# Kernel tuning notes

Measured on AMD Instinct MI355X. Metric: run time of the kernel, lower is better.

The kernel has to match this reference:

```python
import jax, jax.numpy as jnp
import numpy as np

B, T, C, E = 16, 392, 512, 512
E8 = E // 8          # dim_project output
K = T // 2           # top_k / number of sampled positions
RECEPTIVE_FIELD = 2.0


def setup_inputs() -> dict:
    key = jax.random.key(0)
    ks = jax.random.split(key, 6)
    s = 0.03  # trunc_normal std used by the module init
    return {
        "x_in": jax.random.normal(ks[0], (B, T, C), jnp.float32),
        "W_dim": jax.random.normal(ks[1], (E8, E), jnp.float32) * s,
        "b_dim": jnp.zeros((E8,), jnp.float32),
        "W_time": jax.random.normal(ks[2], (T, T * T), jnp.float32) * s,
        "b_time": jnp.zeros((T,), jnp.float32),
        "W_offa": jax.random.normal(ks[3], (K, T), jnp.float32) * s,
        "W_offd": jax.random.normal(ks[4], (K, T), jnp.float32) * s,
    }


def _grid_sample_1d(x, idx_norm):
    """Bilinear 1D sample along last axis of x (b,T,c) at normalized coords
    idx_norm (b,K); padding_mode='border', align_corners=False.
    Equivalent to the module's F.grid_sample on (b,T,c,1) with grid (0, g)."""
    c = x.shape[-1]
    ix = ((idx_norm + 1.0) * c - 1.0) * 0.5          # unnormalize (align_corners=False)
    x0 = jnp.floor(ix)
    w1 = ix - x0                                     # fractional weight
    x0i = jnp.clip(x0.astype(jnp.int32), 0, c - 1)   # border clamp
    x1i = jnp.clip(x0.astype(jnp.int32) + 1, 0, c - 1)
    v0 = jnp.take_along_axis(x, x0i[:, None, :], axis=2)  # (b,T,K)
    v1 = jnp.take_along_axis(x, x1i[:, None, :], axis=2)
    return v0 * (1.0 - w1)[:, None, :] + v1 * w1[:, None, :]


def reference(x_in, W_dim, b_dim, W_time, b_time, W_offa, W_offd):
    b, t, c = x_in.shape
    scaler = 1.0 / E
    # dot-similarity attention map
    xi = jnp.einsum('btc,ec->bte', x_in, W_dim) + b_dim          # (b,t,E8)
    att = jax.nn.softmax(scaler * jnp.einsum('bie,bje->bij', xi, xi), axis=-1)
    # giant time projection: (b, t*t) @ (t*t, t)
    xt = att.reshape(b, t * t) @ W_time.T + b_time               # (b,t)
    off_a = jnp.tanh(xt @ W_offa.T) * RECEPTIVE_FIELD            # (b,K)
    off_d = jnp.tanh(xt @ W_offd.T) * RECEPTIVE_FIELD
    idx_a = jnp.arange(0, t, 2, dtype=jnp.float32)[None, :] + off_a
    idx_d = jnp.arange(1, t + 1, 2, dtype=jnp.float32)[None, :] + off_d
    # normalize_grid: n = K*2 = t
    denom = float(max(t - 1, 1))
    g_a = 2.0 * idx_a / denom - 1.0
    g_d = 2.0 * idx_d / denom - 1.0
    x_a = _grid_sample_1d(x_in, g_a)                             # (b,t,K)
    x_d = _grid_sample_1d(x_in, g_d)
    return (x_a, x_d)
```

## Files before the change

kernel.cpp:

```cpp
#include <hip/hip_runtime.h>
#include <hip/hip_bf16.h>

constexpr int BB   = 16;
constexpr int TT_  = 392;
constexpr int CC   = 512;
constexpr int E8_  = 64;
constexpr int KK   = 196;
constexpr long TT2 = 153664;
constexpr long OUT_HALF = 1229312;

constexpr int NC2 = 98;
constexpr int CH2 = 1568;
constexpr int NJT16 = 25;

constexpr int LDA = 68;

typedef __bf16 bf16_t;
typedef bf16_t bf16x8 __attribute__((ext_vector_type(8)));
typedef float  f32x4  __attribute__((ext_vector_type(4)));

static __device__ __forceinline__ unsigned int pk2(float a, float b) {
    unsigned short lo = __builtin_bit_cast(unsigned short, (bf16_t)a);
    unsigned short hi = __builtin_bit_cast(unsigned short, (bf16_t)b);
    return ((unsigned int)hi << 16) | (unsigned int)lo;
}
static __device__ __forceinline__ bf16x8 cvt8(f32x4 a, f32x4 b) {
    uint4 u = make_uint4(pk2(a.x, a.y), pk2(a.z, a.w), pk2(b.x, b.y), pk2(b.z, b.w));
    return __builtin_bit_cast(bf16x8, u);
}
static __device__ __forceinline__ bf16x8 ld_frag(const bf16_t* p) {
    uint2 lo = *(const uint2*)p;
    uint2 hi = *(const uint2*)(p + 4);
    uint4 u = make_uint4(lo.x, lo.y, hi.x, hi.y);
    return __builtin_bit_cast(bf16x8, u);
}

__global__ __launch_bounds__(256) void k_xi(const float* __restrict__ x,
                                            const float* __restrict__ Wd,
                                            const float* __restrict__ bd,
                                            unsigned short* __restrict__ xi_b,
                                            float* __restrict__ xt) {
    int tid = threadIdx.x;
    if (blockIdx.x < 25) {
        int o = blockIdx.x * 256 + tid;
        if (o < BB * TT_) xt[o] = 0.f;
    }
    int wv = tid >> 6, lane = tid & 63;
    int n = lane & 15, quad = lane >> 4;
    int m = blockIdx.x * 64 + wv * 16 + n;
    const float* xp = x  + (size_t)m * CC + quad * 8;
    const float* wp = Wd + (size_t)n * CC + quad * 8;

    f32x4 acc[4] = {};
    f32x4 a0c, a1c, b0c[4], b1c[4];
    a0c = *(const f32x4*)xp;
    a1c = *(const f32x4*)(xp + 4);
    #pragma unroll
    for (int nt = 0; nt < 4; ++nt) {
        b0c[nt] = *(const f32x4*)(wp + (size_t)nt * 16 * CC);
        b1c[nt] = *(const f32x4*)(wp + (size_t)nt * 16 * CC + 4);
    }
    for (int kt = 0; kt < 16; ++kt) {
        f32x4 a0n, a1n, b0n[4], b1n[4];
        if (kt < 15) {
            a0n = *(const f32x4*)(xp + (kt + 1) * 32);
            a1n = *(const f32x4*)(xp + (kt + 1) * 32 + 4);
            #pragma unroll
            for (int nt = 0; nt < 4; ++nt) {
                b0n[nt] = *(const f32x4*)(wp + (size_t)nt * 16 * CC + (kt + 1) * 32);
                b1n[nt] = *(const f32x4*)(wp + (size_t)nt * 16 * CC + (kt + 1) * 32 + 4);
            }
        }
        bf16x8 a = cvt8(a0c, a1c);
        #pragma unroll
        for (int nt = 0; nt < 4; ++nt) {
            bf16x8 b = cvt8(b0c[nt], b1c[nt]);
            acc[nt] = __builtin_amdgcn_mfma_f32_16x16x32_bf16(a, b, acc[nt], 0, 0, 0);
        }
        if (kt < 15) {
            a0c = a0n; a1c = a1n;
            #pragma unroll
            for (int nt = 0; nt < 4; ++nt) { b0c[nt] = b0n[nt]; b1c[nt] = b1n[nt]; }
        }
    }
    #pragma unroll
    for (int nt = 0; nt < 4; ++nt)
        #pragma unroll
        for (int r = 0; r < 4; ++r) {
            int mm = blockIdx.x * 64 + wv * 16 + quad * 4 + r;
            int e = nt * 16 + n;
            xi_b[(size_t)mm * E8_ + e] =
                __builtin_bit_cast(unsigned short, (bf16_t)(acc[nt][r] + bd[e]));
        }
}

__global__ __launch_bounds__(256) void k_att(const unsigned short* __restrict__ xi_b,
                                             unsigned short* __restrict__ att_b) {
    __shared__ bf16_t Xb[400 * LDA];
    int b = blockIdx.x, tb = blockIdx.y;
    int tid = threadIdx.x;
    int wv = tid >> 6, lane = tid & 63;
    int n = lane & 15, quad = lane >> 4;
    #pragma unroll
    for (int t = 0; t < 13; ++t) {
        int s = t * 256 + tid;
        if (s < 3200) {
            int r = s >> 3, c8 = s & 7;
            uint2 lo = make_uint2(0u, 0u), hi = make_uint2(0u, 0u);
            if (r < TT_) {
                uint4 v = *(const uint4*)(xi_b + ((size_t)(b * TT_ + r)) * E8_ + c8 * 8);
                lo = make_uint2(v.x, v.y);
                hi = make_uint2(v.z, v.w);
            }
            *(uint2*)(&Xb[r * LDA + c8 * 8])     = lo;
            *(uint2*)(&Xb[r * LDA + c8 * 8 + 4]) = hi;
        }
    }
    __syncthreads();
    int arow = tb * 64 + wv * 16 + n;
    if (arow > 399) arow = 399;
    bf16x8 a0 = ld_frag(&Xb[arow * LDA + quad * 8]);
    bf16x8 a1 = ld_frag(&Xb[arow * LDA + 32 + quad * 8]);
    f32x4 acc[25];
    #pragma unroll
    for (int nt = 0; nt < 25; ++nt) acc[nt] = (f32x4){0.f, 0.f, 0.f, 0.f};
    #pragma unroll
    for (int nt = 0; nt < 25; ++nt) {
        bf16x8 b0 = ld_frag(&Xb[(nt * 16 + n) * LDA + quad * 8]);
        bf16x8 b1 = ld_frag(&Xb[(nt * 16 + n) * LDA + 32 + quad * 8]);
        acc[nt] = __builtin_amdgcn_mfma_f32_16x16x32_bf16(a0, b0, acc[nt], 0, 0, 0);
        acc[nt] = __builtin_amdgcn_mfma_f32_16x16x32_bf16(a1, b1, acc[nt], 0, 0, 0);
    }
    const float scaler = 1.0f / 512.0f;
    float mx[4] = {-1e30f, -1e30f, -1e30f, -1e30f};
    #pragma unroll
    for (int nt = 0; nt < 25; ++nt) {
        bool valid = (nt * 16 + n) < TT_;
        #pragma unroll
        for (int r = 0; r < 4; ++r) {
            float v = valid ? acc[nt][r] * scaler : -1e30f;
            acc[nt][r] = v;
            mx[r] = fmaxf(mx[r], v);
        }
    }
    #pragma unroll
    for (int r = 0; r < 4; ++r) {
        #pragma unroll
        for (int o = 1; o < 16; o <<= 1) mx[r] = fmaxf(mx[r], __shfl_xor(mx[r], o, 64));
    }
    float sm[4] = {0.f, 0.f, 0.f, 0.f};
    #pragma unroll
    for (int nt = 0; nt < 25; ++nt)
        #pragma unroll
        for (int r = 0; r < 4; ++r) {
            float e = __expf(acc[nt][r] - mx[r]);
            acc[nt][r] = e;
            sm[r] += e;
        }
    #pragma unroll
    for (int r = 0; r < 4; ++r) {
        #pragma unroll
        for (int o = 1; o < 16; o <<= 1) sm[r] += __shfl_xor(sm[r], o, 64);
        sm[r] = 1.0f / sm[r];
    }
    unsigned short* dst = att_b + (size_t)b * TT2;
    #pragma unroll
    for (int r = 0; r < 4; ++r) {
        int ti = tb * 64 + wv * 16 + quad * 4 + r;
        if (ti < TT_) {
            #pragma unroll
            for (int nt = 0; nt < 25; ++nt) {
                int tj = nt * 16 + n;
                if (tj < TT_)
                    dst[(size_t)ti * TT_ + tj] =
                        __builtin_bit_cast(unsigned short, (bf16_t)(acc[nt][r] * sm[r]));
            }
        }
    }
}

__global__ __launch_bounds__(256) void k_xt(const float* __restrict__ Wt,
                                            const unsigned short* __restrict__ att_b,
                                            float* __restrict__ xt) {
    int wg = blockIdx.x;
    int xcd = wg & 7, s = wg >> 3;
    int cidx = s / 7, jt4 = s - cidx * 7;
    int c = cidx * 8 + xcd;
    if (c >= NC2) return;
    int tid = threadIdx.x;
    int wv = tid >> 6, lane = tid & 63;
    int n = lane & 15, quad = lane >> 4;
    int jt = jt4 * 4 + wv;
    if (jt >= NJT16) return;
    int j = jt * 16 + n;
    int jl = j < TT_ ? j : TT_ - 1;
    long kbase = (long)c * CH2;
    const unsigned short* ap = att_b + (size_t)n * TT2 + kbase + quad * 8;
    const float*          wp = Wt + (size_t)jl * TT2 + kbase + quad * 8;

    f32x4 acc = {0.f, 0.f, 0.f, 0.f};
    uint4 ac; f32x4 w0c, w1c;
    ac  = *(const uint4*)ap;
    w0c = *(const f32x4*)wp;
    w1c = *(const f32x4*)(wp + 4);
    for (int m = 0; m < 49; ++m) {
        uint4 an; f32x4 w0n, w1n;
        if (m < 48) {
            ac.w = ac.w;
            an  = *(const uint4*)(ap + (m + 1) * 32);
            w0n = *(const f32x4*)(wp + (m + 1) * 32);
            w1n = *(const f32x4*)(wp + (m + 1) * 32 + 4);
        }
        bf16x8 a = __builtin_bit_cast(bf16x8, ac);
        bf16x8 b = cvt8(w0c, w1c);
        acc = __builtin_amdgcn_mfma_f32_16x16x32_bf16(a, b, acc, 0, 0, 0);
        if (m < 48) { ac = an; w0c = w0n; w1c = w1n; }
    }
    if (j < TT_) {
        #pragma unroll
        for (int r = 0; r < 4; ++r)
            unsafeAtomicAdd(&xt[(size_t)(quad * 4 + r) * TT_ + j], acc[r]);
    }
}

__global__ __launch_bounds__(256) void k_off(const float* __restrict__ xt,
                                             const float* __restrict__ bt,
                                             const float* __restrict__ Wa,
                                             const float* __restrict__ Wd,
                                             float* __restrict__ wix) {
    int o = blockIdx.x * 256 + threadIdx.x;
    if (o >= 2 * BB * KK) return;
    int which = o / (BB * KK);
    int rem = o - which * (BB * KK);
    int b = rem / KK;
    int k = rem - b * KK;
    const f32x4* __restrict__ wr = (const f32x4*)((which ? Wd : Wa) + (size_t)k * TT_);
    const f32x4* __restrict__ xr = (const f32x4*)(xt + (size_t)b * TT_);
    const f32x4* __restrict__ br = (const f32x4*)bt;
    float acc = 0.f;
    #pragma unroll 2
    for (int q = 0; q < TT_ / 4; ++q) {
        f32x4 w = wr[q], x = xr[q], bb = br[q];
        acc += (x.x + bb.x) * w.x + (x.y + bb.y) * w.y
             + (x.z + bb.z) * w.z + (x.w + bb.w) * w.w;
    }
    float off = tanhf(acc) * 2.0f;
    float idx = (float)(2 * k + which) + off;
    float g = 2.0f * idx / 391.0f - 1.0f;
    float ix = ((g + 1.0f) * 512.0f - 1.0f) * 0.5f;
    wix[o] = ix;
}

__global__ __launch_bounds__(256) void k_sample(const float* __restrict__ x,
                                                const float* __restrict__ wix,
                                                float* __restrict__ out) {
    __shared__ float xr[4][512];
    int b = blockIdx.x, t0 = blockIdx.y * 4;
    int tid = threadIdx.x;
    const float* src = x + ((size_t)b * TT_ + t0) * CC;
    #pragma unroll
    for (int s = 0; s < 2; ++s) {
        int idx = s * 256 + tid;
        ((f32x4*)xr)[idx] = ((const f32x4*)src)[idx];
    }
    __syncthreads();
    for (int w = tid; w < 2 * 4 * KK; w += 256) {
        int which = (w >= 4 * KK) ? 1 : 0;
        int rem = w - which * 4 * KK;
        int tl = rem / KK;
        int k = rem - tl * KK;
        float ix = wix[(size_t)which * (BB * KK) + b * KK + k];
        float x0f = floorf(ix);
        float w1 = ix - x0f;
        int c0 = (int)x0f;
        int c1 = c0 + 1;
        c0 = min(max(c0, 0), CC - 1);
        c1 = min(max(c1, 0), CC - 1);
        float v0 = xr[tl][c0], v1 = xr[tl][c1];
        out[(size_t)which * OUT_HALF + ((size_t)(b * TT_) + t0 + tl) * KK + k] =
            v0 * (1.0f - w1) + v1 * w1;
    }
}

extern "C" void kernel_launch(void* const* d_in, const int* in_sizes, int n_in,
                              void* d_out, int out_size, void* d_ws, size_t ws_size,
                              hipStream_t stream) {
    const float* x_in   = (const float*)d_in[0];
    const float* W_dim  = (const float*)d_in[1];
    const float* b_dim  = (const float*)d_in[2];
    const float* W_time = (const float*)d_in[3];
    const float* b_time = (const float*)d_in[4];
    const float* W_offa = (const float*)d_in[5];
    const float* W_offd = (const float*)d_in[6];
    float* out = (float*)d_out;
    float* ws  = (float*)d_ws;

    unsigned short* att_b = (unsigned short*)ws;
    unsigned short* xi_b  = (unsigned short*)(ws + 1229312);
    float*          xt    = ws + 1630720;
    float*          wix   = ws + 1636992;

    k_xi<<<98, 256, 0, stream>>>(x_in, W_dim, b_dim, xi_b, xt);
    k_att<<<dim3(BB, 7), 256, 0, stream>>>(xi_b, att_b);
    k_xt<<<728, 256, 0, stream>>>(W_time, att_b, xt);
    k_off<<<25, 256, 0, stream>>>(xt, b_time, W_offa, W_offd, wix);
    k_sample<<<dim3(BB, TT_ / 4), 256, 0, stream>>>(x_in, wix, out);
}
```

Measured before the change: 411.8 us.

## Fuse attention softmax into time-projection kernel, recomputing rows in LDS

Removes the separate attention kernel and its global att buffer. Each time-projection workgroup recomputes the softmax rows for its K-chunk across all batches and stages them in shared memory before the W_time MFMA loop. This eliminates the att write and read-back and one launch. In exchange it adds redundant attention compute across column blocks, wastes MFMA rows (only 4 of 16 are used), and uses a large LDS footprint that may reduce occupancy.

```diff
diff --git a/kernel.cpp b/kernel.cpp
--- a/kernel.cpp
+++ b/kernel.cpp
@@ -11,9 +11,7 @@
 
 constexpr int NC2 = 98;
 constexpr int CH2 = 1568;
-constexpr int NJT16 = 25;
-
-constexpr int LDA = 68;
+constexpr int LDP = 1580;
 
 typedef __bf16 bf16_t;
 typedef bf16_t bf16x8 __attribute__((ext_vector_type(8)));
@@ -94,132 +92,110 @@
         }
 }
 
-__global__ __launch_bounds__(256) void k_att(const unsigned short* __restrict__ xi_b,
-                                             unsigned short* __restrict__ att_b) {
-    __shared__ bf16_t Xb[400 * LDA];
-    int b = blockIdx.x, tb = blockIdx.y;
-    int tid = threadIdx.x;
-    int wv = tid >> 6, lane = tid & 63;
-    int n = lane & 15, quad = lane >> 4;
-    #pragma unroll
-    for (int t = 0; t < 13; ++t) {
-        int s = t * 256 + tid;
-        if (s < 3200) {
-            int r = s >> 3, c8 = s & 7;
-            uint2 lo = make_uint2(0u, 0u), hi = make_uint2(0u, 0u);
-            if (r < TT_) {
-                uint4 v = *(const uint4*)(xi_b + ((size_t)(b * TT_ + r)) * E8_ + c8 * 8);
-                lo = make_uint2(v.x, v.y);
-                hi = make_uint2(v.z, v.w);
-            }
-            *(uint2*)(&Xb[r * LDA + c8 * 8])     = lo;
-            *(uint2*)(&Xb[r * LDA + c8 * 8 + 4]) = hi;
-        }
-    }
-    __syncthreads();
-    int arow = tb * 64 + wv * 16 + n;
-    if (arow > 399) arow = 399;
-    bf16x8 a0 = ld_frag(&Xb[arow * LDA + quad * 8]);
-    bf16x8 a1 = ld_frag(&Xb[arow * LDA + 32 + quad * 8]);
-    f32x4 acc[25];
-    #pragma unroll
-    for (int nt = 0; nt < 25; ++nt) acc[nt] = (f32x4){0.f, 0.f, 0.f, 0.f};
-    #pragma unroll
-    for (int nt = 0; nt < 25; ++nt) {
-        bf16x8 b0 = ld_frag(&Xb[(nt * 16 + n) * LDA + quad * 8]);
-        bf16x8 b1 = ld_frag(&Xb[(nt * 16 + n) * LDA + 32 + quad * 8]);
-        acc[nt] = __builtin_amdgcn_mfma_f32_16x16x32_bf16(a0, b0, acc[nt], 0, 0, 0);
-        acc[nt] = __builtin_amdgcn_mfma_f32_16x16x32_bf16(a1, b1, acc[nt], 0, 0, 0);
-    }
-    const float scaler = 1.0f / 512.0f;
-    float mx[4] = {-1e30f, -1e30f, -1e30f, -1e30f};
-    #pragma unroll
-    for (int nt = 0; nt < 25; ++nt) {
-        bool valid = (nt * 16 + n) < TT_;
-        #pragma unroll
-        for (int r = 0; r < 4; ++r) {
-            float v = valid ? acc[nt][r] * scaler : -1e30f;
-            acc[nt][r] = v;
-            mx[r] = fmaxf(mx[r], v);
-        }
-    }
-    #pragma unroll
-    for (int r = 0; r < 4; ++r) {
-        #pragma unroll
-        for (int o = 1; o < 16; o <<= 1) mx[r] = fmaxf(mx[r], __shfl_xor(mx[r], o, 64));
-    }
-    float sm[4] = {0.f, 0.f, 0.f, 0.f};
-    #pragma unroll
-    for (int nt = 0; nt < 25; ++nt)
-        #pragma unroll
-        for (int r = 0; r < 4; ++r) {
-            float e = __expf(acc[nt][r] - mx[r]);
-            acc[nt][r] = e;
-            sm[r] += e;
-        }
-    #pragma unroll
-    for (int r = 0; r < 4; ++r) {
-        #pragma unroll
-        for (int o = 1; o < 16; o <<= 1) sm[r] += __shfl_xor(sm[r], o, 64);
-        sm[r] = 1.0f / sm[r];
-    }
-    unsigned short* dst = att_b + (size_t)b * TT2;
-    #pragma unroll
-    for (int r = 0; r < 4; ++r) {
-        int ti = tb * 64 + wv * 16 + quad * 4 + r;
-        if (ti < TT_) {
-            #pragma unroll
-            for (int nt = 0; nt < 25; ++nt) {
-                int tj = nt * 16 + n;
-                if (tj < TT_)
-                    dst[(size_t)ti * TT_ + tj] =
-                        __builtin_bit_cast(unsigned short, (bf16_t)(acc[nt][r] * sm[r]));
-            }
-        }
-    }
-}
-
-__global__ __launch_bounds__(256) void k_xt(const float* __restrict__ Wt,
-                                            const unsigned short* __restrict__ att_b,
-                                            float* __restrict__ xt) {
+__global__ __launch_bounds__(256) void k_attxt(const float* __restrict__ Wt,
+                                               const unsigned short* __restrict__ xi_b,
+                                               float* __restrict__ xt) {
+    __shared__ bf16_t P[16 * LDP];
     int wg = blockIdx.x;
     int xcd = wg & 7, s = wg >> 3;
-    int cidx = s / 7, jt4 = s - cidx * 7;
+    int cidx = s / 7, jb = s - cidx * 7;
     int c = cidx * 8 + xcd;
     if (c >= NC2) return;
     int tid = threadIdx.x;
     int wv = tid >> 6, lane = tid & 63;
     int n = lane & 15, quad = lane >> 4;
-    int jt = jt4 * 4 + wv;
-    if (jt >= NJT16) return;
-    int j = jt * 16 + n;
+
+    int j = jb * 64 + wv * 16 + n;
     int jl = j < TT_ ? j : TT_ - 1;
     long kbase = (long)c * CH2;
-    const unsigned short* ap = att_b + (size_t)n * TT2 + kbase + quad * 8;
-    const float*          wp = Wt + (size_t)jl * TT2 + kbase + quad * 8;
-
-    f32x4 acc = {0.f, 0.f, 0.f, 0.f};
-    uint4 ac; f32x4 w0c, w1c;
-    ac  = *(const uint4*)ap;
-    w0c = *(const f32x4*)wp;
-    w1c = *(const f32x4*)(wp + 4);
+    const float* wp = Wt + (size_t)jl * TT2 + kbase + quad * 8;
+    f32x4 w0c = *(const f32x4*)wp;
+    f32x4 w1c = *(const f32x4*)(wp + 4);
+
+    const float scaler = 1.0f / 512.0f;
+    for (int bb = 0; bb < 4; ++bb) {
+        int b = wv * 4 + bb;
+        const unsigned short* xb = xi_b + (size_t)b * TT_ * E8_;
+        int ar = 4 * c + (n < 4 ? n : 3);
+        uint4 av0 = *(const uint4*)(xb + (size_t)ar * E8_ + quad * 8);
+        uint4 av1 = *(const uint4*)(xb + (size_t)ar * E8_ + 32 + quad * 8);
+        bf16x8 a0 = __builtin_bit_cast(bf16x8, av0);
+        bf16x8 a1 = __builtin_bit_cast(bf16x8, av1);
+        f32x4 acc[25];
+        #pragma unroll
+        for (int nt = 0; nt < 25; ++nt) acc[nt] = (f32x4){0.f, 0.f, 0.f, 0.f};
+        #pragma unroll
+        for (int nt = 0; nt < 25; ++nt) {
+            int tj = nt * 16 + n;
+            int tjl = tj < TT_ ? tj : TT_ - 1;
+            uint4 bv0 = *(const uint4*)(xb + (size_t)tjl * E8_ + quad * 8);
+            uint4 bv1 = *(const uint4*)(xb + (size_t)tjl * E8_ + 32 + quad * 8);
+            acc[nt] = __builtin_amdgcn_mfma_f32_16x16x32_bf16(
+                a0, __builtin_bit_cast(bf16x8, bv0), acc[nt], 0, 0, 0);
+            acc[nt] = __builtin_amdgcn_mfma_f32_16x16x32_bf16(
+                a1, __builtin_bit_cast(bf16x8, bv1), acc[nt], 0, 0, 0);
+        }
+        float mx[4] = {-1e30f, -1e30f, -1e30f, -1e30f};
+        #pragma unroll
+        for (int nt = 0; nt < 25; ++nt) {
+            bool valid = (nt * 16 + n) < TT_;
+            #pragma unroll
+            for (int r = 0; r < 4; ++r) {
+                float v = valid ? acc[nt][r] * scaler : -1e30f;
+                acc[nt][r] = v;
+                mx[r] = fmaxf(mx[r], v);
+            }
+        }
+        #pragma unroll
+        for (int r = 0; r < 4; ++r) {
+            #pragma unroll
+            for (int o = 1; o < 16; o <<= 1) mx[r] = fmaxf(mx[r], __shfl_xor(mx[r], o, 64));
+        }
+        float sm[4] = {0.f, 0.f, 0.f, 0.f};
+        #pragma unroll
+        for (int nt = 0; nt < 25; ++nt)
+            #pragma unroll
+            for (int r = 0; r < 4; ++r) {
+                float e = __expf(acc[nt][r] - mx[r]);
+                acc[nt][r] = e;
+                sm[r] += e;
+            }
+        #pragma unroll
+        for (int r = 0; r < 4; ++r) {
+            #pragma unroll
+            for (int o = 1; o < 16; o <<= 1) sm[r] += __shfl_xor(sm[r], o, 64);
+            sm[r] = 1.0f / sm[r];
+        }
+        if (quad == 0) {
+            #pragma unroll
+            for (int r = 0; r < 4; ++r)
+                #pragma unroll
+                for (int nt = 0; nt < 25; ++nt) {
+                    int tj = nt * 16 + n;
+                    if (tj < TT_)
+                        P[b * LDP + r * TT_ + tj] = (bf16_t)(acc[nt][r] * sm[r]);
+                }
+        }
+    }
+    __syncthreads();
+
+    const bf16_t* pp = &P[n * LDP + quad * 8];
+    f32x4 acc2 = {0.f, 0.f, 0.f, 0.f};
     for (int m = 0; m < 49; ++m) {
-        uint4 an; f32x4 w0n, w1n;
+        f32x4 w0n, w1n;
         if (m < 48) {
-            ac.w = ac.w;
-            an  = *(const uint4*)(ap + (m + 1) * 32);
             w0n = *(const f32x4*)(wp + (m + 1) * 32);
             w1n = *(const f32x4*)(wp + (m + 1) * 32 + 4);
         }
-        bf16x8 a = __builtin_bit_cast(bf16x8, ac);
+        bf16x8 a = ld_frag(pp + m * 32);
         bf16x8 b = cvt8(w0c, w1c);
-        acc = __builtin_amdgcn_mfma_f32_16x16x32_bf16(a, b, acc, 0, 0, 0);
-        if (m < 48) { ac = an; w0c = w0n; w1c = w1n; }
+        acc2 = __builtin_amdgcn_mfma_f32_16x16x32_bf16(a, b, acc2, 0, 0, 0);
+        if (m < 48) { w0c = w0n; w1c = w1n; }
     }
     if (j < TT_) {
         #pragma unroll
         for (int r = 0; r < 4; ++r)
-            unsafeAtomicAdd(&xt[(size_t)(quad * 4 + r) * TT_ + j], acc[r]);
+            unsafeAtomicAdd(&xt[(size_t)(quad * 4 + r) * TT_ + j], acc2[r]);
     }
 }
 
@@ -295,14 +271,12 @@
     float* out = (float*)d_out;
     float* ws  = (float*)d_ws;
 
-    unsigned short* att_b = (unsigned short*)ws;
-    unsigned short* xi_b  = (unsigned short*)(ws + 1229312);
-    float*          xt    = ws + 1630720;
-    float*          wix   = ws + 1636992;
+    unsigned short* xi_b = (unsigned short*)ws;
+    float*          xt   = ws + 200704;
+    float*          wix  = ws + 206976;
 
     k_xi<<<98, 256, 0, stream>>>(x_in, W_dim, b_dim, xi_b, xt);
-    k_att<<<dim3(BB, 7), 256, 0, stream>>>(xi_b, att_b);
-    k_xt<<<728, 256, 0, stream>>>(W_time, att_b, xt);
+    k_attxt<<<728, 256, 0, stream>>>(W_time, xi_b, xt);
     k_off<<<25, 256, 0, stream>>>(xt, b_time, W_offa, W_offd, wix);
     k_sample<<<dim3(BB, TT_ / 4), 256, 0, stream>>>(x_in, wix, out);
 }
```

Result: slower. 468.5 us (+13.8%).
